# Performance work log

Hardware: AMD Instinct MI355X
Metric: run time of the kernel (lower is better)

Reference implementation:

```python
import jax, jax.numpy as jnp
import numpy as np

SR = 44100
S_TAUS = [10.0, 50.0, 100.0]   # ms
L_TAUS = [500.0, 1500.0, 3000.0]  # ms
EPS = 1e-8


def ms2coef(ms, sr):
    return float(1.0 - np.exp(-2200.0 / (ms * sr)))


def ema(x, coef):
    # First-order leaky integrator y[t] = coef*x[t] + (1-coef)*y[t-1], y[-1]=0.
    # x: [B, T]; scan over time with carry of shape [B].
    coef = jnp.asarray(coef, x.dtype)
    one_m = jnp.asarray(1.0, x.dtype) - coef

    def step(carry, xt):
        y = coef * xt + one_m * carry
        return y, y

    _, ys = jax.lax.scan(step, jnp.zeros(x.shape[0], x.dtype), x.T)
    return ys.T  # [B, T]


def hadamard(x):
    # mid/side transform on channel dim (-2), orthonormal scaling
    m = x[..., 0, :] + x[..., 1, :]
    s = x[..., 0, :] - x[..., 1, :]
    return jnp.stack([m, s], axis=-2) * jnp.asarray(np.sqrt(0.5), x.dtype)


def ldr_feat(x_sq, s_coef, l_coef, shift):
    # log short-term envelope minus (time-aligned) log long-term envelope
    short = jnp.log(ema(x_sq, s_coef))
    long_ = jnp.log(ema(x_sq, l_coef))
    return short - jnp.roll(long_, -shift, axis=-1)


def setup_inputs() -> dict:
    key = jax.random.key(0)
    k1, k2 = jax.random.split(key)
    x_pred = jax.random.normal(k1, (4, 2, 1048576), dtype=jnp.float32)
    x_true = jax.random.normal(k2, (4, 2, 1048576), dtype=jnp.float32)
    return {"x_pred": x_pred, "x_true": x_true}


def reference(x_pred, x_true):
    xp = hadamard(x_pred)
    xt = hadamard(x_true)
    T = xp.shape[-1]
    ps = jnp.clip(jnp.square(xp), EPS, None).reshape(-1, T)
    ts = jnp.clip(jnp.square(xt), EPS, None).reshape(-1, T)
    total = jnp.asarray(0.0, x_pred.dtype)
    for s_ms, l_ms in zip(S_TAUS, L_TAUS):
        sc = ms2coef(s_ms, SR)
        lc = ms2coef(l_ms, SR)
        shift = int(SR * (l_ms - s_ms) * 0.0005)
        fp = ldr_feat(ps, sc, lc, shift)
        ft = ldr_feat(ts, sc, lc, shift)
        total = total + jnp.mean(jnp.abs(fp - ft))
    return total
```

## Files before the change

### kernel.cpp

```cpp
#include <hip/hip_runtime.h>
#include <cmath>


#define T_LEN    1048576
#define CHUNKS   256
#define CLEN     4096
#define NT1      256
#define SEG1     16
#define NT3      256
#define SEG3     16
#define NT4      512
#define SEG4     8
#define COLS     65536
#define JMAX     65535
#define EPS_CLIP 1e-8f
#define K2SEG    32
#define K2NSEG   8

struct K1Args {
  float d[6];
  float a1p[6][8];
};
struct K2Args {
  float dL[6];
  float dL32[6];
};
struct ScanPack {
  float d[3];
  float apw[3][6];
  float A[3];
  int   cis[3];
};

__device__ __constant__ const int D_SHIFT[3] = {10804, 31972, 63945};

__global__ __launch_bounds__(NT1)
void k1_stage(const float* __restrict__ xp, const float* __restrict__ xt,
              float* __restrict__ Eloc, float* __restrict__ Lloc, K1Args ka)
{
  int chunk = blockIdx.x, b = blockIdx.y;
  int which = b >> 2, sig = b & 3, tid = threadIdx.x;
  long base = (long)chunk * CLEN + (long)tid * SEG1;
  const float* x0 = (which ? xt : xp) + (long)sig * 2 * T_LEN;
  const float* x1 = x0 + T_LEN;

  float v[12];
#pragma unroll
  for (int j = 0; j < 12; j++) v[j] = 0.f;

#pragma unroll
  for (int i = 0; i < SEG1 / 4; i++) {
    float4 a = *(const float4*)(x0 + base + 4*i);
    float4 c4 = *(const float4*)(x1 + base + 4*i);
    float sm, sp, pm, ps;
#define STEP(CMP) \
    sm = a.CMP + c4.CMP; sp = a.CMP - c4.CMP; \
    pm = fmaxf(0.5f * sm * sm, EPS_CLIP); ps = fmaxf(0.5f * sp * sp, EPS_CLIP); \
    _Pragma("unroll") \
    for (int cf = 0; cf < 6; cf++) { \
      v[cf*2+0] = fmaf(ka.d[cf], v[cf*2+0], pm); \
      v[cf*2+1] = fmaf(ka.d[cf], v[cf*2+1], ps); \
    }
    STEP(x) STEP(y) STEP(z) STEP(w)
#undef STEP
  }

  {
    long col = (long)chunk * (CLEN / 16) + tid;
#pragma unroll
    for (int k = 0; k < 3; k++) {
      int cf = 2 * k + 1;
#pragma unroll
      for (int st2 = 0; st2 < 2; st2++) {
        long row = (long)(k * 4 + which * 2 + st2);
        Lloc[row * (4L * COLS) + (long)sig * COLS + col] = v[cf * 2 + st2];
      }
    }
  }

  int e = (NT1 - 1) - tid;
  float wv[12];
#pragma unroll
  for (int j = 0; j < 12; j++) {
    float wgt = 1.f;
#pragma unroll
    for (int bb = 0; bb < 8; bb++)
      if (e & (1 << bb)) wgt *= ka.a1p[j >> 1][bb];
    wv[j] = v[j] * wgt;
  }
#pragma unroll
  for (int off = 32; off > 0; off >>= 1)
#pragma unroll
    for (int j = 0; j < 12; j++) wv[j] += __shfl_down(wv[j], off, 64);

  __shared__ float lds[4][12];
  int lane = tid & 63, w = tid >> 6;
  if (lane == 0)
#pragma unroll
    for (int j = 0; j < 12; j++) lds[w][j] = wv[j];
  __syncthreads();
  if (tid < 12) {
    int cf = tid >> 1, st = tid & 1;
    int row = which * 8 + sig * 2 + st;
    Eloc[chunk * 96 + row * 6 + cf] = lds[0][tid] + lds[1][tid] + lds[2][tid] + lds[3][tid];
  }
}

__global__ __launch_bounds__(768)
void k2_scan(const float* __restrict__ Eloc, float* __restrict__ Y, K2Args ka)
{
  int col = threadIdx.x;
  int seg = threadIdx.y;
  float dL = ka.dL[col % 6];
  float A  = ka.dL32[col % 6];
  int c0 = seg * K2SEG;

  float yloc[K2SEG];
  float y = 0.f;
#pragma unroll
  for (int i = 0; i < K2SEG; i++) {
    y = fmaf(dL, y, Eloc[(c0 + i) * 96 + col]);
    yloc[i] = y;
  }

  __shared__ float SY[K2NSEG][96];
  SY[seg][col] = y;
  __syncthreads();

  float C = 0.f;
  for (int s = 0; s < seg; s++) C = fmaf(A, C, SY[s][col]);

  float w = dL;
#pragma unroll
  for (int i = 0; i < K2SEG; i++) {
    Y[(c0 + i) * 96 + col] = fmaf(w, C, yloc[i]);
    w *= dL;
  }
}

__device__ __forceinline__ void scan12(const float v[12], const ScanPack& sp,
                                       const float Yc[12], int tid,
                                       float (*WT)[12], float cin[12])
{
  int lane = tid & 63, w = tid >> 6;
  float S[12];
#pragma unroll
  for (int j = 0; j < 12; j++) S[j] = v[j];
#pragma unroll
  for (int i = 0; i < 6; i++) {
#pragma unroll
    for (int j = 0; j < 12; j++) {
      float up = __shfl_up(S[j], 1u << i, 64);
      if (lane >= (1 << i)) S[j] = fmaf(sp.apw[j >> 2][i], up, S[j]);
    }
  }
  float X[12];
#pragma unroll
  for (int j = 0; j < 12; j++) {
    X[j] = __shfl_up(S[j], 1, 64);
    if (lane == 0) X[j] = 0.f;
  }
  if (lane == 63)
#pragma unroll
    for (int j = 0; j < 12; j++) WT[w][j] = S[j];
  __syncthreads();
  float C[12];
#pragma unroll
  for (int j = 0; j < 12; j++) C[j] = 0.f;
#pragma unroll
  for (int i = 0; i < 8; i++) {
    if (i < w) {
#pragma unroll
      for (int j = 0; j < 12; j++) C[j] = fmaf(sp.A[j >> 2], C[j], WT[i][j]);
    }
  }
  float alane[3], Aw[3];
#pragma unroll
  for (int k = 0; k < 3; k++) {
    float al = 1.f;
#pragma unroll
    for (int i = 0; i < 6; i++)
      if (lane & (1 << i)) al *= sp.apw[k][i];
    alane[k] = al;
    float aw = 1.f, ap = sp.A[k];
#pragma unroll
    for (int i = 0; i < 3; i++) { if (w & (1 << i)) aw *= ap; ap *= ap; }
    Aw[k] = aw;
  }
#pragma unroll
  for (int j = 0; j < 12; j++) {
    int k = j >> 2;
    cin[j] = fmaf(alane[k], fmaf(Aw[k], Yc[j], C[j]), X[j]);
  }
}

__device__ __forceinline__ void loadYc12(const float* __restrict__ Y, int chunk, int sig,
                                         const ScanPack& sp, float Yc[12])
{
#pragma unroll
  for (int j = 0; j < 12; j++) Yc[j] = 0.f;
  if (chunk > 0) {
    const float* Yp = Y + (chunk - 1) * 96;
    int rm = sig * 2;
#pragma unroll
    for (int k = 0; k < 3; k++) {
      int ci = sp.cis[k];
      Yc[4*k+0] = Yp[rm * 6 + ci];       Yc[4*k+1] = Yp[(rm + 1) * 6 + ci];
      Yc[4*k+2] = Yp[(8 + rm) * 6 + ci]; Yc[4*k+3] = Yp[(8 + rm + 1) * 6 + ci];
    }
  }
}

__global__ __launch_bounds__(NT3)
void k3_table(const float* __restrict__ Lloc, const float* __restrict__ Y,
              float* __restrict__ Etab, ScanPack sp)
{
  int chunk = blockIdx.x, sig = blockIdx.y, tid = threadIdx.x;
  long col = (long)chunk * (CLEN / 16) + tid;

  float st[12];
#pragma unroll
  for (int j = 0; j < 12; j++)
    st[j] = Lloc[(long)j * (4L * COLS) + (long)sig * COLS + col];

  float Yc[12];
  loadYc12(Y, chunk, sig, sp, Yc);
  __shared__ float WT[4][12];
  float cin[12];
  scan12(st, sp, Yc, tid, WT, cin);

#pragma unroll
  for (int k = 0; k < 3; k++) {
    float a16 = sp.apw[k][0];
    float y0 = fmaf(a16, cin[4*k+0], st[4*k+0]);
    float y1 = fmaf(a16, cin[4*k+1], st[4*k+1]);
    float y2 = fmaf(a16, cin[4*k+2], st[4*k+2]);
    float y3 = fmaf(a16, cin[4*k+3], st[4*k+3]);
    float em = __logf(__fdividef(y0, y2));
    float es = __logf(__fdividef(y1, y3));
    long rowm = (long)(k * 8 + sig * 2);
    Etab[rowm * COLS + col] = em;
    Etab[(rowm + 1) * COLS + col] = es;
  }
}

__device__ __forceinline__ float slow_lerp(const float* __restrict__ row, int q)
{
  int qm = q - 15;
  if (qm < 0) return row[0];
  int j = qm >> 4;
  if (j >= JMAX) return row[JMAX];
  float f = (float)(qm & 15) * 0.0625f;
  float a = row[j], b = row[j + 1];
  return fmaf(f, b - a, a);
}

__global__ __launch_bounds__(NT4)
void k4all(const float* __restrict__ xp, const float* __restrict__ xt,
           const float* __restrict__ Y, const float* __restrict__ Etab,
           float* __restrict__ part, ScanPack sp)
{
  int chunk = blockIdx.x, sig = blockIdx.y, tid = threadIdx.x;
  long base = (long)chunk * CLEN + (long)tid * SEG4;
  const float* pb = xp + (long)sig * 2 * T_LEN;
  const float* tb = xt + (long)sig * 2 * T_LEN;

  float p[4][SEG4];
  {
    float4 A0 = *(const float4*)(pb + base),         A1 = *(const float4*)(pb + base + 4);
    float4 B0 = *(const float4*)(pb + T_LEN + base), B1 = *(const float4*)(pb + T_LEN + base + 4);
    float4 C0 = *(const float4*)(tb + base),         C1 = *(const float4*)(tb + base + 4);
    float4 D0 = *(const float4*)(tb + T_LEN + base), D1 = *(const float4*)(tb + T_LEN + base + 4);
    float m;
#define QQ(i, AV, BV, CV, DV, CMP) \
    m = AV.CMP + BV.CMP; p[0][i] = fmaxf(0.5f * m * m, EPS_CLIP); \
    m = AV.CMP - BV.CMP; p[1][i] = fmaxf(0.5f * m * m, EPS_CLIP); \
    m = CV.CMP + DV.CMP; p[2][i] = fmaxf(0.5f * m * m, EPS_CLIP); \
    m = CV.CMP - DV.CMP; p[3][i] = fmaxf(0.5f * m * m, EPS_CLIP);
    QQ(0,A0,B0,C0,D0,x) QQ(1,A0,B0,C0,D0,y) QQ(2,A0,B0,C0,D0,z) QQ(3,A0,B0,C0,D0,w)
    QQ(4,A1,B1,C1,D1,x) QQ(5,A1,B1,C1,D1,y) QQ(6,A1,B1,C1,D1,z) QQ(7,A1,B1,C1,D1,w)
#undef QQ
  }

  float tm0[3], tm1[3], tm2[3], ts0[3], ts1[3], ts2[3];
  int ofs[3], q0a[3]; bool fastp[3];
#pragma unroll
  for (int k = 0; k < 3; k++) {
    int q0 = (int)base + D_SHIFT[k]; if (q0 >= T_LEN) q0 -= T_LEN;
    q0a[k] = q0;
    int qm = q0 - 15;
    bool f = (qm >= 0) && ((qm >> 4) <= JMAX - 2);
    fastp[k] = f;
    const float* Tm = Etab + (long)(k * 8 + sig * 2) * COLS;
    const float* Ts = Tm + COLS;
    int j0 = f ? (qm >> 4) : 0;
    ofs[k] = f ? (qm & 15) : 0;
    tm0[k] = Tm[j0]; tm1[k] = Tm[j0 + 1]; tm2[k] = Tm[j0 + 2];
    ts0[k] = Ts[j0]; ts1[k] = Ts[j0 + 1]; ts2[k] = Ts[j0 + 2];
  }

  float st[12];
#pragma unroll
  for (int j = 0; j < 12; j++) st[j] = 0.f;
#pragma unroll
  for (int m = 0; m < SEG4; m++) {
#pragma unroll
    for (int k = 0; k < 3; k++) {
      float dd = sp.d[k];
      st[4*k+0] = fmaf(dd, st[4*k+0], p[0][m]); st[4*k+1] = fmaf(dd, st[4*k+1], p[1][m]);
      st[4*k+2] = fmaf(dd, st[4*k+2], p[2][m]); st[4*k+3] = fmaf(dd, st[4*k+3], p[3][m]);
    }
  }
  float Yc[12];
  loadYc12(Y, chunk, sig, sp, Yc);
  __shared__ float WT[8][12];
  float cin[12];
  scan12(st, sp, Yc, tid, WT, cin);

  float acc0 = 0.f, acc1 = 0.f;
#pragma unroll
  for (int k = 0; k < 3; k++) {
    float d = sp.d[k];
    float y0 = cin[4*k+0], y1 = cin[4*k+1], y2 = cin[4*k+2], y3 = cin[4*k+3];
#pragma unroll
    for (int m = 0; m < SEG4; m++) {
      y0 = fmaf(d, y0, p[0][m]); y1 = fmaf(d, y1, p[1][m]);
      y2 = fmaf(d, y2, p[2][m]); y3 = fmaf(d, y3, p[3][m]);
      float Dm = __logf(__fdividef(y0, y2));
      float Ds = __logf(__fdividef(y1, y3));
      float em, es;
      if (fastp[k]) {
        int d0 = ofs[k] + m;
        bool hi = d0 >= 16;
        float am = hi ? tm1[k] : tm0[k], bm = hi ? tm2[k] : tm1[k];
        float as = hi ? ts1[k] : ts0[k], bs = hi ? ts2[k] : ts1[k];
        float f = (float)(d0 - (hi ? 16 : 0)) * 0.0625f;
        em = fmaf(f, bm - am, am);
        es = fmaf(f, bs - as, as);
      } else {
        int q = q0a[k] + m; if (q >= T_LEN) q -= T_LEN;
        const float* Tm = Etab + (long)(k * 8 + sig * 2) * COLS;
        em = slow_lerp(Tm, q);
        es = slow_lerp(Tm + COLS, q);
      }
      acc0 += fabsf(Dm - em);
      acc1 += fabsf(Ds - es);
    }
  }

  float acc = acc0 + acc1;
#pragma unroll
  for (int off = 32; off > 0; off >>= 1) acc += __shfl_down(acc, off, 64);
  __shared__ float psum[8];
  int lane = tid & 63, w = tid >> 6;
  if (lane == 0) psum[w] = acc;
  __syncthreads();
  if (tid == 0) {
    float s = 0.f;
#pragma unroll
    for (int i = 0; i < 8; i++) s += psum[i];
    part[sig * CHUNKS + chunk] = s;
  }
}

__global__ void k5_final(const float* __restrict__ part, float* __restrict__ out)
{
  __shared__ double lds[256];
  int tid = threadIdx.x;
  double s = 0.0;
  for (int i = tid; i < 4 * CHUNKS; i += 256) s += (double)part[i];
  lds[tid] = s; __syncthreads();
  for (int o = 128; o > 0; o >>= 1) {
    if (tid < o) lds[tid] += lds[tid + o];
    __syncthreads();
  }
  if (tid == 0) out[0] = (float)(lds[0] * (1.0 / (8.0 * 1048576.0)));
}

extern "C" void kernel_launch(void* const* d_in, const int* in_sizes, int n_in,
                              void* d_out, int out_size, void* d_ws, size_t ws_size,
                              hipStream_t stream)
{
  (void)in_sizes; (void)n_in; (void)out_size; (void)ws_size;
  const float* xp = (const float*)d_in[0];
  const float* xt = (const float*)d_in[1];
  float* out = (float*)d_out;
  char* ws = (char*)d_ws;

  const size_t OFF_ELOC = 0;
  const size_t OFF_Y    = 98304;
  const size_t OFF_PART = 196608;
  const size_t OFF_ETAB = 212992;
  const size_t OFF_LLOC = 6504448;
  float* Eloc = (float*)(ws + OFF_ELOC);
  float* Ybuf = (float*)(ws + OFF_Y);
  float* part = (float*)(ws + OFF_PART);
  float* Etab = (float*)(ws + OFF_ETAB);
  float* Lloc = (float*)(ws + OFF_LLOC);

  static const double S_MS[3] = {10.0, 50.0, 100.0};
  static const double L_MS[3] = {500.0, 1500.0, 3000.0};

  K1Args k1a; K2Args k2a; ScanPack spL, spS;
  for (int k = 0; k < 3; k++) {
    for (int which = 0; which < 2; which++) {
      int idx = 2 * k + which;
      double ms = which ? L_MS[k] : S_MS[k];
      float cF = (float)(1.0 - std::exp(-2200.0 / (ms * 44100.0)));
      float dF = 1.0f - cF;
      k1a.d[idx] = dF;
      double a16 = std::pow((double)dF, (double)SEG1);
      for (int b = 0; b < 8; b++)
        k1a.a1p[idx][b] = (float)std::pow(a16, (double)(1 << b));
      k2a.dL[idx] = (float)std::pow((double)dF, (double)CLEN);
      k2a.dL32[idx] = (float)std::pow((double)dF, (double)CLEN * (double)K2SEG);
      ScanPack& sp = which ? spL : spS;
      int seg = which ? SEG3 : SEG4;
      sp.d[k] = dF;
      double aS = std::pow((double)dF, (double)seg);
      for (int i = 0; i < 6; i++)
        sp.apw[k][i] = (float)std::pow(aS, (double)(1 << i));
      sp.A[k] = (float)std::pow(aS, 64.0);
      sp.cis[k] = idx;
    }
  }

  k1_stage<<<dim3(CHUNKS, 8), NT1, 0, stream>>>(xp, xt, Eloc, Lloc, k1a);
  k2_scan<<<dim3(1), dim3(96, K2NSEG), 0, stream>>>(Eloc, Ybuf, k2a);
  k3_table<<<dim3(CHUNKS, 4), NT3, 0, stream>>>(Lloc, Ybuf, Etab, spL);
  k4all<<<dim3(CHUNKS, 4), NT4, 0, stream>>>(xp, xt, Ybuf, Etab, part, spS);
  k5_final<<<1, 256, 0, stream>>>(part, out);
}
```

Baseline: 157.2 us.

## Move intra-chunk scans into stage 1 and drop rescans from table and loss kernels

The first kernel now runs a full block-level prefix scan over its 16-sample segment states, for both short and long coefficients. It stores the per-column carries, and the block total replaces the old weighted reduction. The table kernel and the fused loss kernel then only apply a precomputed decay factor to the chunk carry instead of redoing warp and block scans. The loss kernel uses 256 threads with 16 samples each, log2 differences with the ln2 factor moved into the final reduction, and a fallback path when the workspace is too small. This adds workspace traffic for the short-coefficient carries in exchange for removing duplicated scan work.

```diff
diff --git a/kernel.cpp b/kernel.cpp
--- a/kernel.cpp
+++ b/kernel.cpp
@@ -7,10 +7,6 @@
 #define CLEN     4096
 #define NT1      256
 #define SEG1     16
-#define NT3      256
-#define SEG3     16
-#define NT4      512
-#define SEG4     8
 #define COLS     65536
 #define JMAX     65535
 #define EPS_CLIP 1e-8f
@@ -19,24 +15,23 @@
 
 struct K1Args {
   float d[6];
-  float a1p[6][8];
+  float apw[6][7];
 };
 struct K2Args {
   float dL[6];
   float dL32[6];
 };
-struct ScanPack {
+struct CarryPack {
   float d[3];
-  float apw[3][6];
-  float A[3];
-  int   cis[3];
+  float apw[3][9];
 };
 
 __device__ __constant__ const int D_SHIFT[3] = {10804, 31972, 63945};
 
 __global__ __launch_bounds__(NT1)
 void k1_stage(const float* __restrict__ xp, const float* __restrict__ xt,
-              float* __restrict__ Eloc, float* __restrict__ Lloc, K1Args ka)
+              float* __restrict__ Eloc, float* __restrict__ Bs,
+              float* __restrict__ Bl, int mode, K1Args ka)
 {
   int chunk = blockIdx.x, b = blockIdx.y;
   int which = b >> 2, sig = b & 3, tid = threadIdx.x;
@@ -44,9 +39,9 @@
   const float* x0 = (which ? xt : xp) + (long)sig * 2 * T_LEN;
   const float* x1 = x0 + T_LEN;
 
-  float v[12];
-#pragma unroll
-  for (int j = 0; j < 12; j++) v[j] = 0.f;
+  float S[12];
+#pragma unroll
+  for (int j = 0; j < 12; j++) S[j] = 0.f;
 
 #pragma unroll
   for (int i = 0; i < SEG1 / 4; i++) {
@@ -58,51 +53,72 @@
     pm = fmaxf(0.5f * sm * sm, EPS_CLIP); ps = fmaxf(0.5f * sp * sp, EPS_CLIP); \
     _Pragma("unroll") \
     for (int cf = 0; cf < 6; cf++) { \
-      v[cf*2+0] = fmaf(ka.d[cf], v[cf*2+0], pm); \
-      v[cf*2+1] = fmaf(ka.d[cf], v[cf*2+1], ps); \
+      S[cf*2+0] = fmaf(ka.d[cf], S[cf*2+0], pm); \
+      S[cf*2+1] = fmaf(ka.d[cf], S[cf*2+1], ps); \
     }
     STEP(x) STEP(y) STEP(z) STEP(w)
 #undef STEP
   }
 
-  {
-    long col = (long)chunk * (CLEN / 16) + tid;
-#pragma unroll
-    for (int k = 0; k < 3; k++) {
-      int cf = 2 * k + 1;
-#pragma unroll
-      for (int st2 = 0; st2 < 2; st2++) {
-        long row = (long)(k * 4 + which * 2 + st2);
-        Lloc[row * (4L * COLS) + (long)sig * COLS + col] = v[cf * 2 + st2];
-      }
-    }
-  }
-
-  int e = (NT1 - 1) - tid;
-  float wv[12];
-#pragma unroll
-  for (int j = 0; j < 12; j++) {
-    float wgt = 1.f;
-#pragma unroll
-    for (int bb = 0; bb < 8; bb++)
-      if (e & (1 << bb)) wgt *= ka.a1p[j >> 1][bb];
-    wv[j] = v[j] * wgt;
-  }
-#pragma unroll
-  for (int off = 32; off > 0; off >>= 1)
-#pragma unroll
-    for (int j = 0; j < 12; j++) wv[j] += __shfl_down(wv[j], off, 64);
-
-  __shared__ float lds[4][12];
   int lane = tid & 63, w = tid >> 6;
-  if (lane == 0)
-#pragma unroll
-    for (int j = 0; j < 12; j++) lds[w][j] = wv[j];
+#pragma unroll
+  for (int i = 0; i < 6; i++) {
+#pragma unroll
+    for (int j = 0; j < 12; j++) {
+      float up = __shfl_up(S[j], 1u << i, 64);
+      if (lane >= (1 << i)) S[j] = fmaf(ka.apw[j >> 1][i], up, S[j]);
+    }
+  }
+  __shared__ float WT[4][12];
+  if (lane == 63)
+#pragma unroll
+    for (int j = 0; j < 12; j++) WT[w][j] = S[j];
   __syncthreads();
-  if (tid < 12) {
-    int cf = tid >> 1, st = tid & 1;
-    int row = which * 8 + sig * 2 + st;
-    Eloc[chunk * 96 + row * 6 + cf] = lds[0][tid] + lds[1][tid] + lds[2][tid] + lds[3][tid];
+  float C[12];
+#pragma unroll
+  for (int j = 0; j < 12; j++) C[j] = 0.f;
+#pragma unroll
+  for (int i = 0; i < 4; i++) {
+    if (i < w) {
+#pragma unroll
+      for (int j = 0; j < 12; j++)
+        C[j] = fmaf(ka.apw[j >> 1][6], C[j], WT[i][j]);
+    }
+  }
+  float alp[6];
+#pragma unroll
+  for (int cf = 0; cf < 6; cf++) {
+    int e = lane + 1;
+    float a = 1.f;
+#pragma unroll
+    for (int i = 0; i < 7; i++)
+      if (e & (1 << i)) a *= ka.apw[cf][i];
+    alp[cf] = a;
+  }
+#pragma unroll
+  for (int j = 0; j < 12; j++) S[j] = fmaf(alp[j >> 1], C[j], S[j]);
+
+  long col = (long)chunk * (CLEN / SEG1) + tid;
+  if (mode & 2) {
+#pragma unroll
+    for (int k = 0; k < 3; k++)
+#pragma unroll
+      for (int st2 = 0; st2 < 2; st2++)
+        Bs[(long)(4*k + which*2 + st2) * (4L*COLS) + (long)sig*COLS + col] = S[4*k + st2];
+  }
+  if (mode & 1) {
+#pragma unroll
+    for (int k = 0; k < 3; k++)
+#pragma unroll
+      for (int st2 = 0; st2 < 2; st2++)
+        Bl[(long)(4*k + which*2 + st2) * (4L*COLS) + (long)sig*COLS + col] = S[4*k + 2 + st2];
+  }
+  if (mode != 2 && tid == NT1 - 1) {
+#pragma unroll
+    for (int cf = 0; cf < 6; cf++)
+#pragma unroll
+      for (int st = 0; st < 2; st++)
+        Eloc[chunk * 96 + (which*8 + sig*2 + st) * 6 + cf] = S[cf*2 + st];
   }
 }
 
@@ -138,65 +154,14 @@
   }
 }
 
-__device__ __forceinline__ void scan12(const float v[12], const ScanPack& sp,
-                                       const float Yc[12], int tid,
-                                       float (*WT)[12], float cin[12])
-{
-  int lane = tid & 63, w = tid >> 6;
-  float S[12];
-#pragma unroll
-  for (int j = 0; j < 12; j++) S[j] = v[j];
-#pragma unroll
-  for (int i = 0; i < 6; i++) {
-#pragma unroll
-    for (int j = 0; j < 12; j++) {
-      float up = __shfl_up(S[j], 1u << i, 64);
-      if (lane >= (1 << i)) S[j] = fmaf(sp.apw[j >> 2][i], up, S[j]);
-    }
-  }
-  float X[12];
-#pragma unroll
-  for (int j = 0; j < 12; j++) {
-    X[j] = __shfl_up(S[j], 1, 64);
-    if (lane == 0) X[j] = 0.f;
-  }
-  if (lane == 63)
-#pragma unroll
-    for (int j = 0; j < 12; j++) WT[w][j] = S[j];
-  __syncthreads();
-  float C[12];
-#pragma unroll
-  for (int j = 0; j < 12; j++) C[j] = 0.f;
-#pragma unroll
-  for (int i = 0; i < 8; i++) {
-    if (i < w) {
-#pragma unroll
-      for (int j = 0; j < 12; j++) C[j] = fmaf(sp.A[j >> 2], C[j], WT[i][j]);
-    }
-  }
-  float alane[3], Aw[3];
-#pragma unroll
-  for (int k = 0; k < 3; k++) {
-    float al = 1.f;
-#pragma unroll
-    for (int i = 0; i < 6; i++)
-      if (lane & (1 << i)) al *= sp.apw[k][i];
-    alane[k] = al;
-    float aw = 1.f, ap = sp.A[k];
-#pragma unroll
-    for (int i = 0; i < 3; i++) { if (w & (1 << i)) aw *= ap; ap *= ap; }
-    Aw[k] = aw;
-  }
-#pragma unroll
-  for (int j = 0; j < 12; j++) {
-    int k = j >> 2;
-    cin[j] = fmaf(alane[k], fmaf(Aw[k], Yc[j], C[j]), X[j]);
-  }
-}
-
-__device__ __forceinline__ void loadYc12(const float* __restrict__ Y, int chunk, int sig,
-                                         const ScanPack& sp, float Yc[12])
-{
+__global__ __launch_bounds__(256)
+void k3_table(const float* __restrict__ Bl, const float* __restrict__ Y,
+              float* __restrict__ Etab, CarryPack cp)
+{
+  int chunk = blockIdx.x, sig = blockIdx.y, tid = threadIdx.x;
+  long col = (long)chunk * 256 + tid;
+
+  float Yc[12];
 #pragma unroll
   for (int j = 0; j < 12; j++) Yc[j] = 0.f;
   if (chunk > 0) {
@@ -204,43 +169,32 @@
     int rm = sig * 2;
 #pragma unroll
     for (int k = 0; k < 3; k++) {
-      int ci = sp.cis[k];
-      Yc[4*k+0] = Yp[rm * 6 + ci];       Yc[4*k+1] = Yp[(rm + 1) * 6 + ci];
-      Yc[4*k+2] = Yp[(8 + rm) * 6 + ci]; Yc[4*k+3] = Yp[(8 + rm + 1) * 6 + ci];
-    }
-  }
-}
-
-__global__ __launch_bounds__(NT3)
-void k3_table(const float* __restrict__ Lloc, const float* __restrict__ Y,
-              float* __restrict__ Etab, ScanPack sp)
-{
-  int chunk = blockIdx.x, sig = blockIdx.y, tid = threadIdx.x;
-  long col = (long)chunk * (CLEN / 16) + tid;
-
-  float st[12];
-#pragma unroll
-  for (int j = 0; j < 12; j++)
-    st[j] = Lloc[(long)j * (4L * COLS) + (long)sig * COLS + col];
-
-  float Yc[12];
-  loadYc12(Y, chunk, sig, sp, Yc);
-  __shared__ float WT[4][12];
-  float cin[12];
-  scan12(st, sp, Yc, tid, WT, cin);
-
+      int cf = 2*k + 1;
+      Yc[4*k+0] = Yp[rm*6 + cf];       Yc[4*k+1] = Yp[(rm+1)*6 + cf];
+      Yc[4*k+2] = Yp[(8+rm)*6 + cf];   Yc[4*k+3] = Yp[(8+rm+1)*6 + cf];
+    }
+  }
+  float fac[3];
 #pragma unroll
   for (int k = 0; k < 3; k++) {
-    float a16 = sp.apw[k][0];
-    float y0 = fmaf(a16, cin[4*k+0], st[4*k+0]);
-    float y1 = fmaf(a16, cin[4*k+1], st[4*k+1]);
-    float y2 = fmaf(a16, cin[4*k+2], st[4*k+2]);
-    float y3 = fmaf(a16, cin[4*k+3], st[4*k+3]);
-    float em = __logf(__fdividef(y0, y2));
-    float es = __logf(__fdividef(y1, y3));
-    long rowm = (long)(k * 8 + sig * 2);
+    int e = tid + 1;
+    float a = 1.f;
+#pragma unroll
+    for (int i = 0; i < 9; i++)
+      if (e & (1 << i)) a *= cp.apw[k][i];
+    fac[k] = a;
+  }
+#pragma unroll
+  for (int k = 0; k < 3; k++) {
+    float y0 = fmaf(fac[k], Yc[4*k+0], Bl[(long)(4*k+0)*(4L*COLS) + (long)sig*COLS + col]);
+    float y1 = fmaf(fac[k], Yc[4*k+1], Bl[(long)(4*k+1)*(4L*COLS) + (long)sig*COLS + col]);
+    float y2 = fmaf(fac[k], Yc[4*k+2], Bl[(long)(4*k+2)*(4L*COLS) + (long)sig*COLS + col]);
+    float y3 = fmaf(fac[k], Yc[4*k+3], Bl[(long)(4*k+3)*(4L*COLS) + (long)sig*COLS + col]);
+    float em = __log2f(y0) - __log2f(y2);
+    float es = __log2f(y1) - __log2f(y3);
+    long rowm = (long)(k*8 + sig*2);
     Etab[rowm * COLS + col] = em;
-    Etab[(rowm + 1) * COLS + col] = es;
+    Etab[(rowm+1) * COLS + col] = es;
   }
 }
 
@@ -255,31 +209,48 @@
   return fmaf(f, b - a, a);
 }
 
-__global__ __launch_bounds__(NT4)
+__global__ __launch_bounds__(256, 6)
 void k4all(const float* __restrict__ xp, const float* __restrict__ xt,
-           const float* __restrict__ Y, const float* __restrict__ Etab,
-           float* __restrict__ part, ScanPack sp)
+           const float* __restrict__ Y, const float* __restrict__ Bs,
+           const float* __restrict__ Etab, float* __restrict__ part, CarryPack cp)
 {
   int chunk = blockIdx.x, sig = blockIdx.y, tid = threadIdx.x;
-  long base = (long)chunk * CLEN + (long)tid * SEG4;
-  const float* pb = xp + (long)sig * 2 * T_LEN;
-  const float* tb = xt + (long)sig * 2 * T_LEN;
-
-  float p[4][SEG4];
-  {
-    float4 A0 = *(const float4*)(pb + base),         A1 = *(const float4*)(pb + base + 4);
-    float4 B0 = *(const float4*)(pb + T_LEN + base), B1 = *(const float4*)(pb + T_LEN + base + 4);
-    float4 C0 = *(const float4*)(tb + base),         C1 = *(const float4*)(tb + base + 4);
-    float4 D0 = *(const float4*)(tb + T_LEN + base), D1 = *(const float4*)(tb + T_LEN + base + 4);
-    float m;
-#define QQ(i, AV, BV, CV, DV, CMP) \
-    m = AV.CMP + BV.CMP; p[0][i] = fmaxf(0.5f * m * m, EPS_CLIP); \
-    m = AV.CMP - BV.CMP; p[1][i] = fmaxf(0.5f * m * m, EPS_CLIP); \
-    m = CV.CMP + DV.CMP; p[2][i] = fmaxf(0.5f * m * m, EPS_CLIP); \
-    m = CV.CMP - DV.CMP; p[3][i] = fmaxf(0.5f * m * m, EPS_CLIP);
-    QQ(0,A0,B0,C0,D0,x) QQ(1,A0,B0,C0,D0,y) QQ(2,A0,B0,C0,D0,z) QQ(3,A0,B0,C0,D0,w)
-    QQ(4,A1,B1,C1,D1,x) QQ(5,A1,B1,C1,D1,y) QQ(6,A1,B1,C1,D1,z) QQ(7,A1,B1,C1,D1,w)
-#undef QQ
+  long col = (long)chunk * 256 + tid;
+  long base = col * 16;
+
+  float Yc[12];
+#pragma unroll
+  for (int j = 0; j < 12; j++) Yc[j] = 0.f;
+  if (chunk > 0) {
+    const float* Yp = Y + (chunk - 1) * 96;
+    int rm = sig * 2;
+#pragma unroll
+    for (int k = 0; k < 3; k++) {
+      int cf = 2*k;
+      Yc[4*k+0] = Yp[rm*6 + cf];       Yc[4*k+1] = Yp[(rm+1)*6 + cf];
+      Yc[4*k+2] = Yp[(8+rm)*6 + cf];   Yc[4*k+3] = Yp[(8+rm+1)*6 + cf];
+    }
+  }
+  float y[12];
+  if (tid == 0) {
+#pragma unroll
+    for (int j = 0; j < 12; j++) y[j] = Yc[j];
+  } else {
+    float fac[3];
+#pragma unroll
+    for (int k = 0; k < 3; k++) {
+      float a = 1.f;
+#pragma unroll
+      for (int i = 0; i < 8; i++)
+        if (tid & (1 << i)) a *= cp.apw[k][i];
+      fac[k] = a;
+    }
+#pragma unroll
+    for (int k = 0; k < 3; k++)
+#pragma unroll
+      for (int q = 0; q < 4; q++)
+        y[4*k+q] = fmaf(fac[k], Yc[4*k+q],
+                        Bs[(long)(4*k+q)*(4L*COLS) + (long)sig*COLS + (col-1)]);
   }
 
   float tm0[3], tm1[3], tm2[3], ts0[3], ts1[3], ts2[3];
@@ -299,68 +270,63 @@
     ts0[k] = Ts[j0]; ts1[k] = Ts[j0 + 1]; ts2[k] = Ts[j0 + 2];
   }
 
-  float st[12];
-#pragma unroll
-  for (int j = 0; j < 12; j++) st[j] = 0.f;
-#pragma unroll
-  for (int m = 0; m < SEG4; m++) {
-#pragma unroll
-    for (int k = 0; k < 3; k++) {
-      float dd = sp.d[k];
-      st[4*k+0] = fmaf(dd, st[4*k+0], p[0][m]); st[4*k+1] = fmaf(dd, st[4*k+1], p[1][m]);
-      st[4*k+2] = fmaf(dd, st[4*k+2], p[2][m]); st[4*k+3] = fmaf(dd, st[4*k+3], p[3][m]);
-    }
-  }
-  float Yc[12];
-  loadYc12(Y, chunk, sig, sp, Yc);
-  __shared__ float WT[8][12];
-  float cin[12];
-  scan12(st, sp, Yc, tid, WT, cin);
+  const float* p0 = xp + (long)sig * 2 * T_LEN;
+  const float* p1 = p0 + T_LEN;
+  const float* t0 = xt + (long)sig * 2 * T_LEN;
+  const float* t1 = t0 + T_LEN;
 
   float acc0 = 0.f, acc1 = 0.f;
 #pragma unroll
-  for (int k = 0; k < 3; k++) {
-    float d = sp.d[k];
-    float y0 = cin[4*k+0], y1 = cin[4*k+1], y2 = cin[4*k+2], y3 = cin[4*k+3];
-#pragma unroll
-    for (int m = 0; m < SEG4; m++) {
-      y0 = fmaf(d, y0, p[0][m]); y1 = fmaf(d, y1, p[1][m]);
-      y2 = fmaf(d, y2, p[2][m]); y3 = fmaf(d, y3, p[3][m]);
-      float Dm = __logf(__fdividef(y0, y2));
-      float Ds = __logf(__fdividef(y1, y3));
-      float em, es;
-      if (fastp[k]) {
-        int d0 = ofs[k] + m;
-        bool hi = d0 >= 16;
-        float am = hi ? tm1[k] : tm0[k], bm = hi ? tm2[k] : tm1[k];
-        float as = hi ? ts1[k] : ts0[k], bs = hi ? ts2[k] : ts1[k];
-        float f = (float)(d0 - (hi ? 16 : 0)) * 0.0625f;
-        em = fmaf(f, bm - am, am);
-        es = fmaf(f, bs - as, as);
-      } else {
-        int q = q0a[k] + m; if (q >= T_LEN) q -= T_LEN;
-        const float* Tm = Etab + (long)(k * 8 + sig * 2) * COLS;
-        em = slow_lerp(Tm, q);
-        es = slow_lerp(Tm + COLS, q);
-      }
-      acc0 += fabsf(Dm - em);
-      acc1 += fabsf(Ds - es);
-    }
+  for (int qt = 0; qt < 4; qt++) {
+    float4 a4 = *(const float4*)(p0 + base + 4*qt);
+    float4 b4 = *(const float4*)(p1 + base + 4*qt);
+    float4 u4 = *(const float4*)(t0 + base + 4*qt);
+    float4 w4 = *(const float4*)(t1 + base + 4*qt);
+#define SAMP(CI, CMP) { \
+      const int m = 4*qt + CI; \
+      float sm = a4.CMP + b4.CMP, sd = a4.CMP - b4.CMP; \
+      float pm = fmaxf(0.5f*sm*sm, EPS_CLIP), ps = fmaxf(0.5f*sd*sd, EPS_CLIP); \
+      float em_ = u4.CMP + w4.CMP, ed_ = u4.CMP - w4.CMP; \
+      float qm_ = fmaxf(0.5f*em_*em_, EPS_CLIP), qs_ = fmaxf(0.5f*ed_*ed_, EPS_CLIP); \
+      _Pragma("unroll") \
+      for (int k = 0; k < 3; k++) { \
+        float dd = cp.d[k]; \
+        y[4*k+0] = fmaf(dd, y[4*k+0], pm);  y[4*k+1] = fmaf(dd, y[4*k+1], ps); \
+        y[4*k+2] = fmaf(dd, y[4*k+2], qm_); y[4*k+3] = fmaf(dd, y[4*k+3], qs_); \
+        float Dm = __log2f(y[4*k+0]) - __log2f(y[4*k+2]); \
+        float Ds = __log2f(y[4*k+1]) - __log2f(y[4*k+3]); \
+        float em, es; \
+        if (fastp[k]) { \
+          int d0 = ofs[k] + m; \
+          bool hi = d0 >= 16; \
+          float am = hi ? tm1[k] : tm0[k], bm = hi ? tm2[k] : tm1[k]; \
+          float as = hi ? ts1[k] : ts0[k], bs = hi ? ts2[k] : ts1[k]; \
+          float f = (float)(d0 - (hi ? 16 : 0)) * 0.0625f; \
+          em = fmaf(f, bm - am, am); \
+          es = fmaf(f, bs - as, as); \
+        } else { \
+          int q = q0a[k] + m; if (q >= T_LEN) q -= T_LEN; \
+          const float* Tm = Etab + (long)(k * 8 + sig * 2) * COLS; \
+          em = slow_lerp(Tm, q); \
+          es = slow_lerp(Tm + COLS, q); \
+        } \
+        acc0 += fabsf(Dm - em); \
+        acc1 += fabsf(Ds - es); \
+      } \
+    }
+    SAMP(0,x) SAMP(1,y) SAMP(2,z) SAMP(3,w)
+#undef SAMP
   }
 
   float acc = acc0 + acc1;
 #pragma unroll
   for (int off = 32; off > 0; off >>= 1) acc += __shfl_down(acc, off, 64);
-  __shared__ float psum[8];
+  __shared__ float psum[4];
   int lane = tid & 63, w = tid >> 6;
   if (lane == 0) psum[w] = acc;
   __syncthreads();
-  if (tid == 0) {
-    float s = 0.f;
-#pragma unroll
-    for (int i = 0; i < 8; i++) s += psum[i];
-    part[sig * CHUNKS + chunk] = s;
-  }
+  if (tid == 0)
+    part[sig * CHUNKS + chunk] = psum[0] + psum[1] + psum[2] + psum[3];
 }
 
 __global__ void k5_final(const float* __restrict__ part, float* __restrict__ out)
@@ -374,14 +340,15 @@
     if (tid < o) lds[tid] += lds[tid + o];
     __syncthreads();
   }
-  if (tid == 0) out[0] = (float)(lds[0] * (1.0 / (8.0 * 1048576.0)));
+  if (tid == 0)
+    out[0] = (float)(lds[0] * (0.6931471805599453 / (8.0 * 1048576.0)));
 }
 
 extern "C" void kernel_launch(void* const* d_in, const int* in_sizes, int n_in,
                               void* d_out, int out_size, void* d_ws, size_t ws_size,
                               hipStream_t stream)
 {
-  (void)in_sizes; (void)n_in; (void)out_size; (void)ws_size;
+  (void)in_sizes; (void)n_in; (void)out_size;
   const float* xp = (const float*)d_in[0];
   const float* xt = (const float*)d_in[1];
   float* out = (float*)d_out;
@@ -391,17 +358,20 @@
   const size_t OFF_Y    = 98304;
   const size_t OFF_PART = 196608;
   const size_t OFF_ETAB = 212992;
-  const size_t OFF_LLOC = 6504448;
+  const size_t OFF_B    = 6504448;
+  const size_t HALF_B   = 12L * 4 * COLS * 4;
+  const size_t NEED_FULL = OFF_B + 2 * HALF_B;
   float* Eloc = (float*)(ws + OFF_ELOC);
   float* Ybuf = (float*)(ws + OFF_Y);
   float* part = (float*)(ws + OFF_PART);
   float* Etab = (float*)(ws + OFF_ETAB);
-  float* Lloc = (float*)(ws + OFF_LLOC);
+  float* Bsh  = (float*)(ws + OFF_B);
+  float* Blo  = (float*)(ws + OFF_B + HALF_B);
 
   static const double S_MS[3] = {10.0, 50.0, 100.0};
   static const double L_MS[3] = {500.0, 1500.0, 3000.0};
 
-  K1Args k1a; K2Args k2a; ScanPack spL, spS;
+  K1Args k1a; K2Args k2a; CarryPack cpS, cpL;
   for (int k = 0; k < 3; k++) {
     for (int which = 0; which < 2; which++) {
       int idx = 2 * k + which;
@@ -409,25 +379,30 @@
       float cF = (float)(1.0 - std::exp(-2200.0 / (ms * 44100.0)));
       float dF = 1.0f - cF;
       k1a.d[idx] = dF;
-      double a16 = std::pow((double)dF, (double)SEG1);
-      for (int b = 0; b < 8; b++)
-        k1a.a1p[idx][b] = (float)std::pow(a16, (double)(1 << b));
-      k2a.dL[idx] = (float)std::pow((double)dF, (double)CLEN);
+      double a16 = std::pow((double)dF, 16.0);
+      for (int i = 0; i < 7; i++)
+        k1a.apw[idx][i] = (float)std::pow(a16, (double)(1 << i));
+      k2a.dL[idx]   = (float)std::pow((double)dF, (double)CLEN);
       k2a.dL32[idx] = (float)std::pow((double)dF, (double)CLEN * (double)K2SEG);
-      ScanPack& sp = which ? spL : spS;
-      int seg = which ? SEG3 : SEG4;
-      sp.d[k] = dF;
-      double aS = std::pow((double)dF, (double)seg);
-      for (int i = 0; i < 6; i++)
-        sp.apw[k][i] = (float)std::pow(aS, (double)(1 << i));
-      sp.A[k] = (float)std::pow(aS, 64.0);
-      sp.cis[k] = idx;
-    }
-  }
-
-  k1_stage<<<dim3(CHUNKS, 8), NT1, 0, stream>>>(xp, xt, Eloc, Lloc, k1a);
-  k2_scan<<<dim3(1), dim3(96, K2NSEG), 0, stream>>>(Eloc, Ybuf, k2a);
-  k3_table<<<dim3(CHUNKS, 4), NT3, 0, stream>>>(Lloc, Ybuf, Etab, spL);
-  k4all<<<dim3(CHUNKS, 4), NT4, 0, stream>>>(xp, xt, Ybuf, Etab, part, spS);
+      CarryPack& cp = which ? cpL : cpS;
+      cp.d[k] = dF;
+      for (int i = 0; i < 9; i++)
+        cp.apw[k][i] = (float)std::pow(a16, (double)(1 << i));
+    }
+  }
+
+  bool full = (ws_size >= NEED_FULL);
+  if (full) {
+    k1_stage<<<dim3(CHUNKS, 8), NT1, 0, stream>>>(xp, xt, Eloc, Bsh, Blo, 3, k1a);
+    k2_scan<<<dim3(1), dim3(96, K2NSEG), 0, stream>>>(Eloc, Ybuf, k2a);
+    k3_table<<<dim3(CHUNKS, 4), 256, 0, stream>>>(Blo, Ybuf, Etab, cpL);
+    k4all<<<dim3(CHUNKS, 4), 256, 0, stream>>>(xp, xt, Ybuf, Bsh, Etab, part, cpS);
+  } else {
+    k1_stage<<<dim3(CHUNKS, 8), NT1, 0, stream>>>(xp, xt, Eloc, Bsh, Bsh, 1, k1a);
+    k2_scan<<<dim3(1), dim3(96, K2NSEG), 0, stream>>>(Eloc, Ybuf, k2a);
+    k3_table<<<dim3(CHUNKS, 4), 256, 0, stream>>>(Bsh, Ybuf, Etab, cpL);
+    k1_stage<<<dim3(CHUNKS, 8), NT1, 0, stream>>>(xp, xt, Eloc, Bsh, Bsh, 2, k1a);
+    k4all<<<dim3(CHUNKS, 4), 256, 0, stream>>>(xp, xt, Ybuf, Bsh, Etab, part, cpS);
+  }
   k5_final<<<1, 256, 0, stream>>>(part, out);
 }
```

Result: slower. 236.6 us (+50.6%).
